# Optimization experiments

Hardware: AMD Instinct MI355X
Metric: run time of the kernel (lower is better)

The kernel has to match this reference:

```python
import jax, jax.numpy as jnp
import numpy as np

# Each of the 16 soft binary logic ops is a polynomial c0 + c1*a + c2*b + c3*a*b.
# Rows below are the [c0, c1, c2, c3] coefficients for ops 0..15 (same math as bin_op).
_OP_COEF = np.array([
    [0., 0., 0., 0.],   # 0: zeros
    [0., 0., 0., 1.],   # 1: a*b
    [0., 1., 0., -1.],  # 2: a - a*b
    [0., 1., 0., 0.],   # 3: a
    [0., 0., 1., -1.],  # 4: b - a*b
    [0., 0., 1., 0.],   # 5: b
    [0., 1., 1., -2.],  # 6: a + b - 2ab
    [0., 1., 1., -1.],  # 7: a + b - ab
    [1., -1., -1., 1.], # 8: 1 - (a + b - ab)
    [1., -1., -1., 2.], # 9: 1 - (a + b - 2ab)
    [1., 0., -1., 0.],  # 10: 1 - b
    [1., 0., -1., 1.],  # 11: 1 - b + ab
    [1., -1., 0., 0.],  # 12: 1 - a
    [1., -1., 0., 1.],  # 13: 1 - a + ab
    [1., 0., 0., -1.],  # 14: 1 - a*b
    [1., 0., 0., 0.],   # 15: ones
], dtype=np.float32)

K_CLASSES = 10
TAU = 30.0


def logic_layer(x, w, idx_a, idx_b):
    # x: [B, in_dim], w: [out_dim, 16], idx_a/idx_b: [out_dim]
    probs = jax.nn.softmax(w, axis=-1)                 # [O, 16]
    coef = probs @ jnp.asarray(_OP_COEF)               # [O, 4]
    a = x[:, idx_a]                                    # [B, O]
    b = x[:, idx_b]                                    # [B, O]
    # weighted mixture of 16 ops == polynomial in (1, a, b, a*b)
    return coef[:, 0] + coef[:, 1] * a + coef[:, 2] * b + coef[:, 3] * (a * b)


def group_sum(x, k, tau):
    B = x.shape[0]
    return x.reshape(B, k, x.shape[-1] // k).sum(-1) / tau


def setup_inputs() -> dict:
    key = jax.random.key(0)
    ks = jax.random.split(key, 10)
    B, D0, D1, D2, D3 = 4096, 1024, 8192, 8192, 10240
    return {
        "x": jax.random.uniform(ks[0], (B, D0), dtype=jnp.float32),
        "w1": jax.random.normal(ks[1], (D1, 16), dtype=jnp.float32),
        "w2": jax.random.normal(ks[2], (D2, 16), dtype=jnp.float32),
        "w3": jax.random.normal(ks[3], (D3, 16), dtype=jnp.float32),
        "idx_a1": jax.random.randint(ks[4], (D1,), 0, D0, dtype=jnp.int32),
        "idx_b1": jax.random.randint(ks[5], (D1,), 0, D0, dtype=jnp.int32),
        "idx_a2": jax.random.randint(ks[6], (D2,), 0, D1, dtype=jnp.int32),
        "idx_b2": jax.random.randint(ks[7], (D2,), 0, D1, dtype=jnp.int32),
        "idx_a3": jax.random.randint(ks[8], (D3,), 0, D2, dtype=jnp.int32),
        "idx_b3": jax.random.randint(ks[9], (D3,), 0, D2, dtype=jnp.int32),
    }


def reference(x, w1, w2, w3, idx_a1, idx_b1, idx_a2, idx_b2, idx_a3, idx_b3):
    h = logic_layer(x, w1, idx_a1, idx_b1)
    h = logic_layer(h, w2, idx_a2, idx_b2)
    h = logic_layer(h, w3, idx_a3, idx_b3)
    return group_sum(h, K_CLASSES, TAU)   # [B, 10]
```

## Files before the change

### kernel.cpp

```cpp
#include <hip/hip_runtime.h>
#include <hip/hip_fp16.h>
#include <stdint.h>

#define D0 1024
#define D1 8192
#define D2 8192
#define D3 10240
#define B_ROWS 4096

#define SM_XB     0
#define SM_H2     16384
#define SM_CSUM   (16384 + 131072)
#define SM_BYTES  (16384 + 131072 + 320)

__device__ __forceinline__ float4 softmax_coef(const float* __restrict__ w) {
    const float4* wv = (const float4*)w;
    float4 q0 = wv[0], q1 = wv[1], q2 = wv[2], q3 = wv[3];
    float wa[16] = {q0.x, q0.y, q0.z, q0.w, q1.x, q1.y, q1.z, q1.w,
                    q2.x, q2.y, q2.z, q2.w, q3.x, q3.y, q3.z, q3.w};
    float m = wa[0];
#pragma unroll
    for (int i = 1; i < 16; ++i) m = fmaxf(m, wa[i]);
    float e[16], s = 0.f;
#pragma unroll
    for (int i = 0; i < 16; ++i) { e[i] = __expf(wa[i] - m); s += e[i]; }
    float inv = 1.f / s;
    static constexpr float OPC[16][4] = {
        {0.f, 0.f, 0.f, 0.f}, {0.f, 0.f, 0.f, 1.f}, {0.f, 1.f, 0.f, -1.f}, {0.f, 1.f, 0.f, 0.f},
        {0.f, 0.f, 1.f, -1.f}, {0.f, 0.f, 1.f, 0.f}, {0.f, 1.f, 1.f, -2.f}, {0.f, 1.f, 1.f, -1.f},
        {1.f, -1.f, -1.f, 1.f}, {1.f, -1.f, -1.f, 2.f}, {1.f, 0.f, -1.f, 0.f}, {1.f, 0.f, -1.f, 1.f},
        {1.f, -1.f, 0.f, 0.f}, {1.f, -1.f, 0.f, 1.f}, {1.f, 0.f, 0.f, -1.f}, {1.f, 0.f, 0.f, 0.f}};
    float c0 = 0.f, c1 = 0.f, c2 = 0.f, c3 = 0.f;
#pragma unroll
    for (int i = 0; i < 16; ++i) {
        float p = e[i] * inv;
        c0 += p * OPC[i][0];
        c1 += p * OPC[i][1];
        c2 += p * OPC[i][2];
        c3 += p * OPC[i][3];
    }
    return make_float4(c0, c1, c2, c3);
}

__device__ __forceinline__ uint2 pack_coef(float4 c) {
    uint2 r;
    r.x = __builtin_bit_cast(uint32_t, __floats2half2_rn(c.x, c.y));
    r.y = __builtin_bit_cast(uint32_t, __floats2half2_rn(c.z, c.w));
    return r;
}

#define PREP_TOTAL (3 * D2 + D3)
__global__ __launch_bounds__(256) void prep_kernel(
    const float* __restrict__ w1, const float* __restrict__ w2,
    const float* __restrict__ w3,
    const int* __restrict__ ia1, const int* __restrict__ ib1,
    const int* __restrict__ ia2, const int* __restrict__ ib2,
    const int* __restrict__ ia3, const int* __restrict__ ib3,
    uint4* __restrict__ bcM1, uint4* __restrict__ bcM2,
    uint4* __restrict__ d3M) {
    int G = blockIdx.x * 256 + threadIdx.x;
    if (G < D2) {
        int g = G;
        int pa = ia2[g], pb = ib2[g];
        float4 cO = softmax_coef(w2 + (size_t)g * 16);
        uint32_t xiA = (uint32_t)(ia1[pa] << 4) | ((uint32_t)(ib1[pa] << 4) << 16);
        uint32_t xiB = (uint32_t)(ia1[pb] << 4) | ((uint32_t)(ib1[pb] << 4) << 16);
        uint2 o = pack_coef(cO);
        bcM1[g] = make_uint4(xiA, xiB, o.x, o.y);
    } else if (G < 2 * D2) {
        int g = G - D2;
        int pa = ia2[g];
        uint2 a = pack_coef(softmax_coef(w1 + (size_t)pa * 16));
        ((uint2*)bcM2)[2 * g] = a;
    } else if (G < 3 * D2) {
        int g = G - 2 * D2;
        int pb = ib2[g];
        uint2 b = pack_coef(softmax_coef(w1 + (size_t)pb * 16));
        ((uint2*)bcM2)[2 * g + 1] = b;
    } else {
        int g = G - 3 * D2;
        float4 cO = softmax_coef(w3 + (size_t)g * 16);
        uint2 o = pack_coef(cO);
        uint32_t ei = (uint32_t)ia3[g] | ((uint32_t)ib3[g] << 16);
        d3M[g] = make_uint4(ei, o.x, o.y, 0u);
    }
}

__device__ __forceinline__ uint4 gate8(uint4 av, uint4 bv, uint2 cf) {
    __half2 p = __builtin_bit_cast(__half2, cf.x);
    __half2 q = __builtin_bit_cast(__half2, cf.y);
    __half2 c0 = __low2half2(p), c1 = __high2half2(p);
    __half2 c2 = __low2half2(q), c3 = __high2half2(q);
    uint4 r;
#pragma unroll
    for (int i = 0; i < 4; ++i) {
        __half2 a = __builtin_bit_cast(__half2, (&av.x)[i]);
        __half2 b = __builtin_bit_cast(__half2, (&bv.x)[i]);
        __half2 h = __hfma2(a, __hfma2(b, c3, c1), __hfma2(b, c2, c0));
        (&r.x)[i] = __builtin_bit_cast(uint32_t, h);
    }
    return r;
}

__device__ __forceinline__ float dpp_sum_f32(float x) {
#define DPPADD(ctrl, rmask)                                              \
    x += __builtin_bit_cast(float, __builtin_amdgcn_update_dpp(          \
             0, __builtin_bit_cast(int, x), (ctrl), (rmask), 0xf, true))
    DPPADD(0x111, 0xf);
    DPPADD(0x112, 0xf);
    DPPADD(0x114, 0xf);
    DPPADD(0x118, 0xf);
    DPPADD(0x142, 0xa);
    DPPADD(0x143, 0xc);
#undef DPPADD
    return x;
}

__device__ __forceinline__ void stage_bc(char* sm, int t,
                                         const uint4* __restrict__ bcM1,
                                         const uint4* __restrict__ bcM2,
                                         uint4 m1a_n, uint4 m1b_n) {
#pragma unroll
    for (int k = 0; k < 4; ++k) {
        uint4 m1a = m1a_n, m1b = m1b_n;
        int g0 = t + (k << 11);
        int g1 = g0 + 1024;
        uint4 m2a = bcM2[g0];
        uint4 m2b = bcM2[g1];
        if (k < 3) {
            m1a_n = bcM1[g0 + 2048];
            m1b_n = bcM1[g1 + 2048];
        }
        uint4 aa0 = *(const uint4*)(sm + (m1a.x & 0xffffu));
        uint4 ab0 = *(const uint4*)(sm + (m1a.x >> 16));
        uint4 ba0 = *(const uint4*)(sm + (m1a.y & 0xffffu));
        uint4 bb0 = *(const uint4*)(sm + (m1a.y >> 16));
        uint4 aa1 = *(const uint4*)(sm + (m1b.x & 0xffffu));
        uint4 ab1 = *(const uint4*)(sm + (m1b.x >> 16));
        uint4 ba1 = *(const uint4*)(sm + (m1b.y & 0xffffu));
        uint4 bb1 = *(const uint4*)(sm + (m1b.y >> 16));
        uint4 h0 = gate8(gate8(aa0, ab0, make_uint2(m2a.x, m2a.y)),
                         gate8(ba0, bb0, make_uint2(m2a.z, m2a.w)),
                         make_uint2(m1a.z, m1a.w));
        uint4 h1v = gate8(gate8(aa1, ab1, make_uint2(m2b.x, m2b.y)),
                          gate8(ba1, bb1, make_uint2(m2b.z, m2b.w)),
                          make_uint2(m1b.z, m1b.w));
        *(uint4*)(sm + SM_H2 + ((uint32_t)g0 << 4)) = h0;
        *(uint4*)(sm + SM_H2 + ((uint32_t)g1 << 4)) = h1v;
    }
}

__device__ __forceinline__ void stage_d(char* sm, int t,
                                        const uint4* __restrict__ d3M,
                                        float* csum) {
    const int wv = t >> 6, lane = t & 63;
    const int gbase = wv * 640;
    const int cA = gbase >> 10;
    const int bnd = (cA + 1) << 10;
    const bool cross = (gbase + 640 > bnd);
    float s0[8] = {0.f, 0.f, 0.f, 0.f, 0.f, 0.f, 0.f, 0.f};
    float s1[8] = {0.f, 0.f, 0.f, 0.f, 0.f, 0.f, 0.f, 0.f};
#pragma unroll
    for (int j = 0; j < 5; ++j) {
        int gc = gbase + (j << 7);
        uint4 ma = d3M[gc + lane];
        uint4 mb = d3M[gc + 64 + lane];
        uint4 av0 = *(const uint4*)(sm + SM_H2 + ((ma.x & 0xffffu) << 4));
        uint4 bv0 = *(const uint4*)(sm + SM_H2 + ((ma.x >> 16) << 4));
        uint4 av1 = *(const uint4*)(sm + SM_H2 + ((mb.x & 0xffffu) << 4));
        uint4 bv1 = *(const uint4*)(sm + SM_H2 + ((mb.x >> 16) << 4));
        uint4 h0 = gate8(av0, bv0, make_uint2(ma.y, ma.z));
        uint4 h1v = gate8(av1, bv1, make_uint2(mb.y, mb.z));
        float pr8[8];
#pragma unroll
        for (int i = 0; i < 4; ++i) {
            __half2 pr = __hadd2(__builtin_bit_cast(__half2, (&h0.x)[i]),
                                 __builtin_bit_cast(__half2, (&h1v.x)[i]));
            pr8[2 * i] = __low2float(pr);
            pr8[2 * i + 1] = __high2float(pr);
        }
        if (gc < bnd) {
#pragma unroll
            for (int r = 0; r < 8; ++r) s0[r] += pr8[r];
        } else {
#pragma unroll
            for (int r = 0; r < 8; ++r) s1[r] += pr8[r];
        }
    }
#pragma unroll
    for (int r = 0; r < 8; ++r) s0[r] = dpp_sum_f32(s0[r]);
    if (cross) {
#pragma unroll
        for (int r = 0; r < 8; ++r) s1[r] = dpp_sum_f32(s1[r]);
    }
    if (lane == 63) {
#pragma unroll
        for (int r = 0; r < 8; ++r) atomicAdd(&csum[cA * 8 + r], s0[r]);
        if (cross) {
#pragma unroll
            for (int r = 0; r < 8; ++r) atomicAdd(&csum[(cA + 1) * 8 + r], s1[r]);
        }
    }
}

__global__ __launch_bounds__(1024, 4) void fused_kernel(
    const float* __restrict__ x, const uint4* __restrict__ bcM1,
    const uint4* __restrict__ bcM2, const uint4* __restrict__ d3M,
    float* __restrict__ out) {
    extern __shared__ char sm[];
    uint4* xb = (uint4*)(sm + SM_XB);
    float* csum = (float*)(sm + SM_CSUM);

    const int t = threadIdx.x;
    const int rowbase = blockIdx.x << 4;

    uint4 m1a_n = bcM1[t];
    uint4 m1b_n = bcM1[t + 1024];

    const float* xp = x + (size_t)rowbase * D0 + t;
    float x2r[8];
#pragma unroll
    for (int i = 0; i < 8; ++i) x2r[i] = xp[(size_t)(8 + i) * D0];
    {
        uint4 v;
#pragma unroll
        for (int i = 0; i < 4; ++i) {
            float va = xp[(size_t)(2 * i) * D0];
            float vb = xp[(size_t)(2 * i + 1) * D0];
            (&v.x)[i] = __builtin_bit_cast(uint32_t, __floats2half2_rn(va, vb));
        }
        xb[t] = v;
    }
    if (t < 80) csum[t] = 0.f;
    __syncthreads();

    stage_bc(sm, t, bcM1, bcM2, m1a_n, m1b_n);
    __syncthreads();

    {
        uint4 v;
#pragma unroll
        for (int i = 0; i < 4; ++i)
            (&v.x)[i] = __builtin_bit_cast(
                uint32_t, __floats2half2_rn(x2r[2 * i], x2r[2 * i + 1]));
        xb[t] = v;
    }
    m1a_n = bcM1[t];
    m1b_n = bcM1[t + 1024];

    stage_d(sm, t, d3M, csum);
    __syncthreads();

    if (t < 80) {
        int c = t >> 3, r = t & 7;
        out[(size_t)(rowbase + r) * 10 + c] = csum[t] * (1.0f / 30.0f);
        csum[t] = 0.f;
    }

    stage_bc(sm, t, bcM1, bcM2, m1a_n, m1b_n);
    __syncthreads();

    stage_d(sm, t, d3M, csum);
    __syncthreads();

    if (t < 80) {
        int c = t >> 3, r = t & 7;
        out[(size_t)(rowbase + 8 + r) * 10 + c] = csum[t] * (1.0f / 30.0f);
    }
}

extern "C" void kernel_launch(void* const* d_in, const int* in_sizes, int n_in,
                              void* d_out, int out_size, void* d_ws, size_t ws_size,
                              hipStream_t stream) {
    const float* x = (const float*)d_in[0];
    const float* w1 = (const float*)d_in[1];
    const float* w2 = (const float*)d_in[2];
    const float* w3 = (const float*)d_in[3];
    const int* ia1 = (const int*)d_in[4];
    const int* ib1 = (const int*)d_in[5];
    const int* ia2 = (const int*)d_in[6];
    const int* ib2 = (const int*)d_in[7];
    const int* ia3 = (const int*)d_in[8];
    const int* ib3 = (const int*)d_in[9];
    float* out = (float*)d_out;

    char* p = (char*)d_ws;
    uint4* bcM1 = (uint4*)p;    p += (size_t)D2 * 16;
    uint4* bcM2 = (uint4*)p;    p += (size_t)D2 * 16;
    uint4* d3M = (uint4*)p;

    hipFuncSetAttribute(reinterpret_cast<const void*>(fused_kernel),
                        hipFuncAttributeMaxDynamicSharedMemorySize, SM_BYTES);

    prep_kernel<<<PREP_TOTAL / 256, 256, 0, stream>>>(
        w1, w2, w3, ia1, ib1, ia2, ib2, ia3, ib3, bcM1, bcM2, d3M);
    fused_kernel<<<B_ROWS / 16, 1024, SM_BYTES, stream>>>(x, bcM1, bcM2, d3M, out);
}
```

Baseline: 98.92 us.

## Merge prep kernel into fused kernel using cooperative launch and grid sync

Folds the coefficient/index precompute kernel into the main fused kernel. Each of the 256 blocks computes 136 prep entries, then a cooperative grid-wide sync separates prep from the main stages. The x loads are issued before prep so their latency overlaps it. This removes one kernel launch and the gap between launches, but adds a grid barrier and a cooperative launch, and relies on all 256 blocks of 1024 threads with large LDS being co-resident.

Result: slower. 218.3 us (+120.7%).

```diff
diff --git a/kernel.cpp b/kernel.cpp
--- a/kernel.cpp
+++ b/kernel.cpp
@@ -1,6 +1,9 @@
 #include <hip/hip_runtime.h>
 #include <hip/hip_fp16.h>
+#include <hip/hip_cooperative_groups.h>
 #include <stdint.h>
+
+namespace cg = cooperative_groups;
 
 #define D0 1024
 #define D1 8192
@@ -12,6 +15,9 @@
 #define SM_H2     16384
 #define SM_CSUM   (16384 + 131072)
 #define SM_BYTES  (16384 + 131072 + 320)
+
+#define PREP_TOTAL (3 * D2 + D3)
+#define PREP_PER_BLOCK 136
 
 __device__ __forceinline__ float4 softmax_coef(const float* __restrict__ w) {
     const float4* wv = (const float4*)w;
@@ -47,43 +53,6 @@
     r.x = __builtin_bit_cast(uint32_t, __floats2half2_rn(c.x, c.y));
     r.y = __builtin_bit_cast(uint32_t, __floats2half2_rn(c.z, c.w));
     return r;
-}
-
-#define PREP_TOTAL (3 * D2 + D3)
-__global__ __launch_bounds__(256) void prep_kernel(
-    const float* __restrict__ w1, const float* __restrict__ w2,
-    const float* __restrict__ w3,
-    const int* __restrict__ ia1, const int* __restrict__ ib1,
-    const int* __restrict__ ia2, const int* __restrict__ ib2,
-    const int* __restrict__ ia3, const int* __restrict__ ib3,
-    uint4* __restrict__ bcM1, uint4* __restrict__ bcM2,
-    uint4* __restrict__ d3M) {
-    int G = blockIdx.x * 256 + threadIdx.x;
-    if (G < D2) {
-        int g = G;
-        int pa = ia2[g], pb = ib2[g];
-        float4 cO = softmax_coef(w2 + (size_t)g * 16);
-        uint32_t xiA = (uint32_t)(ia1[pa] << 4) | ((uint32_t)(ib1[pa] << 4) << 16);
-        uint32_t xiB = (uint32_t)(ia1[pb] << 4) | ((uint32_t)(ib1[pb] << 4) << 16);
-        uint2 o = pack_coef(cO);
-        bcM1[g] = make_uint4(xiA, xiB, o.x, o.y);
-    } else if (G < 2 * D2) {
-        int g = G - D2;
-        int pa = ia2[g];
-        uint2 a = pack_coef(softmax_coef(w1 + (size_t)pa * 16));
-        ((uint2*)bcM2)[2 * g] = a;
-    } else if (G < 3 * D2) {
-        int g = G - 2 * D2;
-        int pb = ib2[g];
-        uint2 b = pack_coef(softmax_coef(w1 + (size_t)pb * 16));
-        ((uint2*)bcM2)[2 * g + 1] = b;
-    } else {
-        int g = G - 3 * D2;
-        float4 cO = softmax_coef(w3 + (size_t)g * 16);
-        uint2 o = pack_coef(cO);
-        uint32_t ei = (uint32_t)ia3[g] | ((uint32_t)ib3[g] << 16);
-        d3M[g] = make_uint4(ei, o.x, o.y, 0u);
-    }
 }
 
 __device__ __forceinline__ uint4 gate8(uint4 av, uint4 bv, uint2 cf) {
@@ -203,10 +172,15 @@
     }
 }
 
-__global__ __launch_bounds__(1024, 4) void fused_kernel(
-    const float* __restrict__ x, const uint4* __restrict__ bcM1,
-    const uint4* __restrict__ bcM2, const uint4* __restrict__ d3M,
-    float* __restrict__ out) {
+__global__ __launch_bounds__(1024, 4) void fused_all(
+    const float* __restrict__ x,
+    const float* __restrict__ w1, const float* __restrict__ w2,
+    const float* __restrict__ w3,
+    const int* __restrict__ ia1, const int* __restrict__ ib1,
+    const int* __restrict__ ia2, const int* __restrict__ ib2,
+    const int* __restrict__ ia3, const int* __restrict__ ib3,
+    uint4* __restrict__ bcM1, uint4* __restrict__ bcM2,
+    uint4* __restrict__ d3M, float* __restrict__ out) {
     extern __shared__ char sm[];
     uint4* xb = (uint4*)(sm + SM_XB);
     float* csum = (float*)(sm + SM_CSUM);
@@ -214,25 +188,57 @@
     const int t = threadIdx.x;
     const int rowbase = blockIdx.x << 4;
 
+    const float* xp = x + (size_t)rowbase * D0 + t;
+    float x1r[8], x2r[8];
+#pragma unroll
+    for (int i = 0; i < 8; ++i) x1r[i] = xp[(size_t)i * D0];
+#pragma unroll
+    for (int i = 0; i < 8; ++i) x2r[i] = xp[(size_t)(8 + i) * D0];
+
+    if (t < PREP_PER_BLOCK) {
+        int T = blockIdx.x * PREP_PER_BLOCK + t;
+        if (T < D2) {
+            int g = T;
+            int pa = ia2[g], pb = ib2[g];
+            float4 cO = softmax_coef(w2 + (size_t)g * 16);
+            uint32_t xiA = (uint32_t)(ia1[pa] << 4) | ((uint32_t)(ib1[pa] << 4) << 16);
+            uint32_t xiB = (uint32_t)(ia1[pb] << 4) | ((uint32_t)(ib1[pb] << 4) << 16);
+            uint2 o = pack_coef(cO);
+            bcM1[g] = make_uint4(xiA, xiB, o.x, o.y);
+        } else if (T < 2 * D2) {
+            int g = T - D2;
+            int pa = ia2[g];
+            uint2 a = pack_coef(softmax_coef(w1 + (size_t)pa * 16));
+            ((uint2*)bcM2)[2 * g] = a;
+        } else if (T < 3 * D2) {
+            int g = T - 2 * D2;
+            int pb = ib2[g];
+            uint2 b = pack_coef(softmax_coef(w1 + (size_t)pb * 16));
+            ((uint2*)bcM2)[2 * g + 1] = b;
+        } else {
+            int g = T - 3 * D2;
+            float4 cO = softmax_coef(w3 + (size_t)g * 16);
+            uint2 o = pack_coef(cO);
+            uint32_t ei = (uint32_t)ia3[g] | ((uint32_t)ib3[g] << 16);
+            d3M[g] = make_uint4(ei, o.x, o.y, 0u);
+        }
+    }
+
+    {
+        uint4 v;
+#pragma unroll
+        for (int i = 0; i < 4; ++i)
+            (&v.x)[i] = __builtin_bit_cast(
+                uint32_t, __floats2half2_rn(x1r[2 * i], x1r[2 * i + 1]));
+        xb[t] = v;
+    }
+    if (t < 80) csum[t] = 0.f;
+
+    __threadfence();
+    cg::this_grid().sync();
+
     uint4 m1a_n = bcM1[t];
     uint4 m1b_n = bcM1[t + 1024];
-
-    const float* xp = x + (size_t)rowbase * D0 + t;
-    float x2r[8];
-#pragma unroll
-    for (int i = 0; i < 8; ++i) x2r[i] = xp[(size_t)(8 + i) * D0];
-    {
-        uint4 v;
-#pragma unroll
-        for (int i = 0; i < 4; ++i) {
-            float va = xp[(size_t)(2 * i) * D0];
-            float vb = xp[(size_t)(2 * i + 1) * D0];
-            (&v.x)[i] = __builtin_bit_cast(uint32_t, __floats2half2_rn(va, vb));
-        }
-        xb[t] = v;
-    }
-    if (t < 80) csum[t] = 0.f;
-    __syncthreads();
 
     stage_bc(sm, t, bcM1, bcM2, m1a_n, m1b_n);
     __syncthreads();
@@ -289,10 +295,14 @@
     uint4* bcM2 = (uint4*)p;    p += (size_t)D2 * 16;
     uint4* d3M = (uint4*)p;
 
-    hipFuncSetAttribute(reinterpret_cast<const void*>(fused_kernel),
+    hipFuncSetAttribute(reinterpret_cast<const void*>(fused_all),
                         hipFuncAttributeMaxDynamicSharedMemorySize, SM_BYTES);
 
-    prep_kernel<<<PREP_TOTAL / 256, 256, 0, stream>>>(
-        w1, w2, w3, ia1, ib1, ia2, ib2, ia3, ib3, bcM1, bcM2, d3M);
-    fused_kernel<<<B_ROWS / 16, 1024, SM_BYTES, stream>>>(x, bcM1, bcM2, d3M, out);
-}
+    void* args[] = {(void*)&x,   (void*)&w1,  (void*)&w2,  (void*)&w3,
+                    (void*)&ia1, (void*)&ib1, (void*)&ia2, (void*)&ib2,
+                    (void*)&ia3, (void*)&ib3, (void*)&bcM1, (void*)&bcM2,
+                    (void*)&d3M, (void*)&out};
+    hipLaunchCooperativeKernel(reinterpret_cast<const void*>(fused_all),
+                               dim3(B_ROWS / 16), dim3(1024), args, SM_BYTES,
+                               stream);
+}
```

## Split softmax prep across quad lanes and skew per-wave gather order

Applied to the files above, without the earlier changes.

The prep kernel now uses four threads per gate, each handling a float4 of the weights and combining max, sum and coefficient partials with xor shuffles, which spreads the serial softmax work over more threads. The fused kernel rotates the order in which each wave walks the bcM1/bcM2 and d3M chunks by a per-wave skew, so concurrent waves touch different cache lines and LDS regions. In exchange, prep launches four times the threads and pays extra shuffle overhead, and the skewed indexing adds a little address arithmetic.

Result: no change. 99.26 us (+0.3%).

```diff
diff --git a/kernel.cpp b/kernel.cpp
--- a/kernel.cpp
+++ b/kernel.cpp
@@ -13,32 +13,32 @@
 #define SM_CSUM   (16384 + 131072)
 #define SM_BYTES  (16384 + 131072 + 320)
 
-__device__ __forceinline__ float4 softmax_coef(const float* __restrict__ w) {
-    const float4* wv = (const float4*)w;
-    float4 q0 = wv[0], q1 = wv[1], q2 = wv[2], q3 = wv[3];
-    float wa[16] = {q0.x, q0.y, q0.z, q0.w, q1.x, q1.y, q1.z, q1.w,
-                    q2.x, q2.y, q2.z, q2.w, q3.x, q3.y, q3.z, q3.w};
-    float m = wa[0];
-#pragma unroll
-    for (int i = 1; i < 16; ++i) m = fmaxf(m, wa[i]);
-    float e[16], s = 0.f;
-#pragma unroll
-    for (int i = 0; i < 16; ++i) { e[i] = __expf(wa[i] - m); s += e[i]; }
+#define PREP_TOTAL (3 * D2 + D3)
+
+__device__ __forceinline__ float4 softmax_coef_quad(
+    const float* __restrict__ w, int q) {
+    float4 v = ((const float4*)w)[q];
+    float m = fmaxf(fmaxf(v.x, v.y), fmaxf(v.z, v.w));
+    m = fmaxf(m, __shfl_xor(m, 1, 64));
+    m = fmaxf(m, __shfl_xor(m, 2, 64));
+    float e0 = __expf(v.x - m), e1 = __expf(v.y - m);
+    float e2 = __expf(v.z - m), e3 = __expf(v.w - m);
+    float s = e0 + e1 + e2 + e3;
+    s += __shfl_xor(s, 1, 64);
+    s += __shfl_xor(s, 2, 64);
     float inv = 1.f / s;
-    static constexpr float OPC[16][4] = {
-        {0.f, 0.f, 0.f, 0.f}, {0.f, 0.f, 0.f, 1.f}, {0.f, 1.f, 0.f, -1.f}, {0.f, 1.f, 0.f, 0.f},
-        {0.f, 0.f, 1.f, -1.f}, {0.f, 0.f, 1.f, 0.f}, {0.f, 1.f, 1.f, -2.f}, {0.f, 1.f, 1.f, -1.f},
-        {1.f, -1.f, -1.f, 1.f}, {1.f, -1.f, -1.f, 2.f}, {1.f, 0.f, -1.f, 0.f}, {1.f, 0.f, -1.f, 1.f},
-        {1.f, -1.f, 0.f, 0.f}, {1.f, -1.f, 0.f, 1.f}, {1.f, 0.f, 0.f, -1.f}, {1.f, 0.f, 0.f, 0.f}};
-    float c0 = 0.f, c1 = 0.f, c2 = 0.f, c3 = 0.f;
-#pragma unroll
-    for (int i = 0; i < 16; ++i) {
-        float p = e[i] * inv;
-        c0 += p * OPC[i][0];
-        c1 += p * OPC[i][1];
-        c2 += p * OPC[i][2];
-        c3 += p * OPC[i][3];
-    }
+    float p0 = e0 * inv, p1 = e1 * inv, p2 = e2 * inv, p3 = e3 * inv;
+    float c0, c1, c2, c3;
+    switch (q) {
+      case 0:  c0 = 0.f;               c1 = p2 + p3;   c2 = 0.f;                 c3 = p1 - p2;              break;
+      case 1:  c0 = 0.f;               c1 = p2 + p3;   c2 = p0 + p1 + p2 + p3;   c3 = -p0 - 2.f * p2 - p3;  break;
+      case 2:  c0 = p0 + p1 + p2 + p3; c1 = -p0 - p1;  c2 = -(p0 + p1 + p2 + p3);c3 = p0 + 2.f * p1 + p3;   break;
+      default: c0 = p0 + p1 + p2 + p3; c1 = -p0 - p1;  c2 = 0.f;                 c3 = p1 - p2;              break;
+    }
+    c0 += __shfl_xor(c0, 1, 64); c0 += __shfl_xor(c0, 2, 64);
+    c1 += __shfl_xor(c1, 1, 64); c1 += __shfl_xor(c1, 2, 64);
+    c2 += __shfl_xor(c2, 1, 64); c2 += __shfl_xor(c2, 2, 64);
+    c3 += __shfl_xor(c3, 1, 64); c3 += __shfl_xor(c3, 2, 64);
     return make_float4(c0, c1, c2, c3);
 }
 
@@ -49,7 +49,6 @@
     return r;
 }
 
-#define PREP_TOTAL (3 * D2 + D3)
 __global__ __launch_bounds__(256) void prep_kernel(
     const float* __restrict__ w1, const float* __restrict__ w2,
     const float* __restrict__ w3,
@@ -58,31 +57,50 @@
     const int* __restrict__ ia3, const int* __restrict__ ib3,
     uint4* __restrict__ bcM1, uint4* __restrict__ bcM2,
     uint4* __restrict__ d3M) {
-    int G = blockIdx.x * 256 + threadIdx.x;
-    if (G < D2) {
-        int g = G;
+    int tid = blockIdx.x * 256 + threadIdx.x;
+    int T = tid >> 2;
+    int q = tid & 3;
+    int lane = threadIdx.x & 63;
+    int qbase = lane & ~3;
+
+    if (T < D2) {
+        int g = T;
         int pa = ia2[g], pb = ib2[g];
-        float4 cO = softmax_coef(w2 + (size_t)g * 16);
-        uint32_t xiA = (uint32_t)(ia1[pa] << 4) | ((uint32_t)(ib1[pa] << 4) << 16);
-        uint32_t xiB = (uint32_t)(ia1[pb] << 4) | ((uint32_t)(ib1[pb] << 4) << 16);
-        uint2 o = pack_coef(cO);
-        bcM1[g] = make_uint4(xiA, xiB, o.x, o.y);
-    } else if (G < 2 * D2) {
-        int g = G - D2;
+        int myi;
+        switch (q) {
+          case 0:  myi = ia1[pa]; break;
+          case 1:  myi = ib1[pa]; break;
+          case 2:  myi = ia1[pb]; break;
+          default: myi = ib1[pb]; break;
+        }
+        uint32_t sh = (uint32_t)(myi << 4);
+        uint32_t i0 = __shfl(sh, qbase + 0, 64);
+        uint32_t i1 = __shfl(sh, qbase + 1, 64);
+        uint32_t i2 = __shfl(sh, qbase + 2, 64);
+        uint32_t i3 = __shfl(sh, qbase + 3, 64);
+        float4 cO = softmax_coef_quad(w2 + (size_t)g * 16, q);
+        if (q == 0) {
+            uint2 o = pack_coef(cO);
+            bcM1[g] = make_uint4(i0 | (i1 << 16), i2 | (i3 << 16), o.x, o.y);
+        }
+    } else if (T < 2 * D2) {
+        int g = T - D2;
         int pa = ia2[g];
-        uint2 a = pack_coef(softmax_coef(w1 + (size_t)pa * 16));
-        ((uint2*)bcM2)[2 * g] = a;
-    } else if (G < 3 * D2) {
-        int g = G - 2 * D2;
+        float4 cA = softmax_coef_quad(w1 + (size_t)pa * 16, q);
+        if (q == 0) ((uint2*)bcM2)[2 * g] = pack_coef(cA);
+    } else if (T < 3 * D2) {
+        int g = T - 2 * D2;
         int pb = ib2[g];
-        uint2 b = pack_coef(softmax_coef(w1 + (size_t)pb * 16));
-        ((uint2*)bcM2)[2 * g + 1] = b;
+        float4 cB = softmax_coef_quad(w1 + (size_t)pb * 16, q);
+        if (q == 0) ((uint2*)bcM2)[2 * g + 1] = pack_coef(cB);
     } else {
-        int g = G - 3 * D2;
-        float4 cO = softmax_coef(w3 + (size_t)g * 16);
-        uint2 o = pack_coef(cO);
-        uint32_t ei = (uint32_t)ia3[g] | ((uint32_t)ib3[g] << 16);
-        d3M[g] = make_uint4(ei, o.x, o.y, 0u);
+        int g = T - 3 * D2;
+        float4 cO = softmax_coef_quad(w3 + (size_t)g * 16, q);
+        if (q == 0) {
+            uint2 o = pack_coef(cO);
+            uint32_t ei = (uint32_t)ia3[g] | ((uint32_t)ib3[g] << 16);
+            d3M[g] = make_uint4(ei, o.x, o.y, 0u);
+        }
     }
 }
 
@@ -116,20 +134,22 @@
     return x;
 }
 
-__device__ __forceinline__ void stage_bc(char* sm, int t,
+__device__ __forceinline__ void stage_bc(char* sm, int t, int skew,
                                          const uint4* __restrict__ bcM1,
                                          const uint4* __restrict__ bcM2,
                                          uint4 m1a_n, uint4 m1b_n) {
 #pragma unroll
     for (int k = 0; k < 4; ++k) {
+        int kk = (k + skew) & 3;
         uint4 m1a = m1a_n, m1b = m1b_n;
-        int g0 = t + (k << 11);
+        int g0 = t + (kk << 11);
         int g1 = g0 + 1024;
         uint4 m2a = bcM2[g0];
         uint4 m2b = bcM2[g1];
         if (k < 3) {
-            m1a_n = bcM1[g0 + 2048];
-            m1b_n = bcM1[g1 + 2048];
+            int kn = (k + 1 + skew) & 3;
+            m1a_n = bcM1[t + (kn << 11)];
+            m1b_n = bcM1[t + (kn << 11) + 1024];
         }
         uint4 aa0 = *(const uint4*)(sm + (m1a.x & 0xffffu));
         uint4 ab0 = *(const uint4*)(sm + (m1a.x >> 16));
@@ -150,7 +170,7 @@
     }
 }
 
-__device__ __forceinline__ void stage_d(char* sm, int t,
+__device__ __forceinline__ void stage_d(char* sm, int t, int skew5,
                                         const uint4* __restrict__ d3M,
                                         float* csum) {
     const int wv = t >> 6, lane = t & 63;
@@ -162,7 +182,8 @@
     float s1[8] = {0.f, 0.f, 0.f, 0.f, 0.f, 0.f, 0.f, 0.f};
 #pragma unroll
     for (int j = 0; j < 5; ++j) {
-        int gc = gbase + (j << 7);
+        int jj = j + skew5; if (jj >= 5) jj -= 5;
+        int gc = gbase + (jj << 7);
         uint4 ma = d3M[gc + lane];
         uint4 mb = d3M[gc + 64 + lane];
         uint4 av0 = *(const uint4*)(sm + SM_H2 + ((ma.x & 0xffffu) << 4));
@@ -212,10 +233,13 @@
     float* csum = (float*)(sm + SM_CSUM);
 
     const int t = threadIdx.x;
+    const int wv = t >> 6;
+    const int skew = wv & 3;
+    const int skew5 = wv % 5;
     const int rowbase = blockIdx.x << 4;
 
-    uint4 m1a_n = bcM1[t];
-    uint4 m1b_n = bcM1[t + 1024];
+    uint4 m1a_n = bcM1[t + (skew << 11)];
+    uint4 m1b_n = bcM1[t + (skew << 11) + 1024];
 
     const float* xp = x + (size_t)rowbase * D0 + t;
     float x2r[8];
@@ -234,7 +258,7 @@
     if (t < 80) csum[t] = 0.f;
     __syncthreads();
 
-    stage_bc(sm, t, bcM1, bcM2, m1a_n, m1b_n);
+    stage_bc(sm, t, skew, bcM1, bcM2, m1a_n, m1b_n);
     __syncthreads();
 
     {
@@ -245,10 +269,10 @@
                 uint32_t, __floats2half2_rn(x2r[2 * i], x2r[2 * i + 1]));
         xb[t] = v;
     }
-    m1a_n = bcM1[t];
-    m1b_n = bcM1[t + 1024];
-
-    stage_d(sm, t, d3M, csum);
+    m1a_n = bcM1[t + (skew << 11)];
+    m1b_n = bcM1[t + (skew << 11) + 1024];
+
+    stage_d(sm, t, skew5, d3M, csum);
     __syncthreads();
 
     if (t < 80) {
@@ -257,10 +281,10 @@
         csum[t] = 0.f;
     }
 
-    stage_bc(sm, t, bcM1, bcM2, m1a_n, m1b_n);
-    __syncthreads();
-
-    stage_d(sm, t, d3M, csum);
+    stage_bc(sm, t, skew, bcM1, bcM2, m1a_n, m1b_n);
+    __syncthreads();
+
+    stage_d(sm, t, skew5, d3M, csum);
     __syncthreads();
 
     if (t < 80) {
@@ -292,7 +316,7 @@
     hipFuncSetAttribute(reinterpret_cast<const void*>(fused_kernel),
                         hipFuncAttributeMaxDynamicSharedMemorySize, SM_BYTES);
 
-    prep_kernel<<<PREP_TOTAL / 256, 256, 0, stream>>>(
+    prep_kernel<<<(4 * PREP_TOTAL) / 256, 256, 0, stream>>>(
         w1, w2, w3, ia1, ib1, ia2, ib2, ia3, ib3, bcM1, bcM2, d3M);
     fused_kernel<<<B_ROWS / 16, 1024, SM_BYTES, stream>>>(x, bcM1, bcM2, d3M, out);
 }
```
